# Kernel optimization log

Measured on AMD Instinct MI355X. Metric: run time of the kernel, lower is better.

The kernel has to match this reference:

```python
import jax, jax.numpy as jnp
import numpy as np

N = 50000      # nodes
E = 800000     # edges (avg degree 16)
D = 128        # in_dim == hidden_dim
CD = 3         # coord_dim (SE(3))
L = 3          # num_layers


def setup_inputs() -> dict:
    key = jax.random.key(0)
    ks = jax.random.split(key, 10)
    s = np.float32(1.0 / np.sqrt(D))
    return {
        "x": jax.random.normal(ks[0], (N, D), jnp.float32),
        "pos": jax.random.normal(ks[1], (N, CD), jnp.float32),
        "edge_index": jax.random.randint(ks[2], (2, E), 0, N, dtype=jnp.int32),
        # per-layer stacked params (in_dim == hidden_dim so all layers stack)
        "Wl": jax.random.normal(ks[3], (L, D, D), jnp.float32) * s,
        "bl": jnp.zeros((L, D), jnp.float32),
        "Wc": jax.random.normal(ks[4], (L, D, 1), jnp.float32) * s,
        "bc": jnp.zeros((L, 1), jnp.float32),
        "WR": jax.random.normal(ks[5], (L, D, CD * CD), jnp.float32) * s,
        "bR": jnp.zeros((L, CD * CD), jnp.float32),
        "Wt": jax.random.normal(ks[6], (L, D, CD), jnp.float32) * s,
        "bt": jnp.zeros((L, CD), jnp.float32),
        # final fc
        "Wf": jax.random.normal(ks[7], (D, D), jnp.float32) * s,
        "bf": jnp.zeros((D,), jnp.float32),
    }


def reference(x, pos, edge_index, Wl, bl, Wc, bc, WR, bR, Wt, bt, Wf, bf):
    src, dst = edge_index[0], edge_index[1]
    n = x.shape[0]
    # R defaults to identity, t to zeros (R_dict/t_dict None path)
    R = jnp.broadcast_to(jnp.eye(CD, dtype=x.dtype), (n, CD, CD))
    t = jnp.zeros_like(pos)
    for i in range(L):
        h = x @ Wl[i] + bl[i]                          # (N, D)  per-edge-type linear
        # MessagePassing aggr='add': message x_j = h[src], scatter-add at dst
        out = jax.ops.segment_sum(h[src], dst, num_segments=n)  # (N, D)
        pos = pos + (out @ Wc[i] + bc[i])              # (N,3) + (N,1) broadcast
        R_upd = (out @ WR[i] + bR[i]).reshape(n, CD, CD)
        Q = jnp.linalg.qr(R_upd)[0]                    # orthonormalize rotation update
        R = Q @ R
        t = t + (out @ Wt[i] + bt[i])
        x = out
    z = x @ Wf + bf
    return z, pos, R, t
```

## Files before the change

### kernel.cpp

```cpp
#include <hip/hip_runtime.h>
#include <hip/hip_fp16.h>

typedef _Float16 half8 __attribute__((ext_vector_type(8)));
typedef float floatx4 __attribute__((ext_vector_type(4)));

#define NHC 16
#define WCOLS (128 + NHC)
#define OSH 13

__device__ inline void qr3_q(const double A[3][3], double Q[3][3]){
  double a[3][3];
#pragma unroll
  for (int r = 0; r < 3; r++)
#pragma unroll
    for (int c = 0; c < 3; c++) a[r][c] = A[r][c];

  double v1[3] = {1.0, 0.0, 0.0};
  double tau1 = 0.0;
  {
    double xn2 = a[1][0]*a[1][0] + a[2][0]*a[2][0];
    if (xn2 != 0.0){
      double alpha = a[0][0];
      double beta = -copysign(sqrt(alpha*alpha + xn2), alpha);
      tau1 = (beta - alpha) / beta;
      double inv = 1.0 / (alpha - beta);
      v1[1] = a[1][0] * inv;
      v1[2] = a[2][0] * inv;
#pragma unroll
      for (int c = 1; c < 3; c++){
        double w = a[0][c] + v1[1]*a[1][c] + v1[2]*a[2][c];
        double tw = tau1 * w;
        a[0][c] -= tw;
        a[1][c] -= tw * v1[1];
        a[2][c] -= tw * v1[2];
      }
    }
  }
  double tau2 = 0.0, v2 = 0.0;
  {
    double x2 = a[2][1];
    if (x2 != 0.0){
      double alpha = a[1][1];
      double beta = -copysign(sqrt(alpha*alpha + x2*x2), alpha);
      tau2 = (beta - alpha) / beta;
      v2 = x2 / (alpha - beta);
    }
  }
  double M[3][3] = {{1.0, 0.0, 0.0},
                    {0.0, 1.0 - tau2, -tau2*v2},
                    {0.0, -tau2*v2, 1.0 - tau2*v2*v2}};
#pragma unroll
  for (int c = 0; c < 3; c++){
    double w = v1[0]*M[0][c] + v1[1]*M[1][c] + v1[2]*M[2][c];
#pragma unroll
    for (int r = 0; r < 3; r++)
      Q[r][c] = M[r][c] - tau1 * v1[r] * w;
  }
}

__device__ inline void se3_node(int n, const float* __restrict__ dsws,
                                const float* __restrict__ bc, const float* __restrict__ bR,
                                const float* __restrict__ bt, const float* __restrict__ pos_in,
                                float* __restrict__ pos_o, float* __restrict__ R_o,
                                float* __restrict__ t_o, int layer, int N){
  float ds[13];
#pragma unroll
  for (int c = 0; c < 13; c++) ds[c] = dsws[(size_t)c*N + n];

  double A[3][3], Q[3][3];
#pragma unroll
  for (int r = 0; r < 3; r++)
#pragma unroll
    for (int c = 0; c < 3; c++)
      A[r][c] = (double)ds[1 + r*3 + c] + (double)bR[r*3 + c];
  qr3_q(A, Q);

  double pd = (double)ds[0] + (double)bc[0];
#pragma unroll
  for (int c = 0; c < 3; c++){
    double base = (layer == 0) ? (double)pos_in[n*3 + c] : (double)pos_o[n*3 + c];
    pos_o[n*3 + c] = (float)(base + pd);
  }

  if (layer == 0){
#pragma unroll
    for (int r = 0; r < 3; r++)
#pragma unroll
      for (int c = 0; c < 3; c++)
        R_o[n*9 + r*3 + c] = (float)Q[r][c];
  } else {
    double Rold[3][3];
#pragma unroll
    for (int r = 0; r < 3; r++)
#pragma unroll
      for (int c = 0; c < 3; c++)
        Rold[r][c] = (double)R_o[n*9 + r*3 + c];
#pragma unroll
    for (int r = 0; r < 3; r++)
#pragma unroll
      for (int c = 0; c < 3; c++){
        double s = Q[r][0]*Rold[0][c] + Q[r][1]*Rold[1][c] + Q[r][2]*Rold[2][c];
        R_o[n*9 + r*3 + c] = (float)s;
      }
  }
#pragma unroll
  for (int c = 0; c < 3; c++){
    double base = (layer == 0) ? 0.0 : (double)t_o[n*3 + c];
    t_o[n*3 + c] = (float)(base + (double)ds[10 + c] + (double)bt[c]);
  }
}

__global__ void k_prep_w(const float* __restrict__ Wl, const float* __restrict__ Wf,
                         const float* __restrict__ Wc, const float* __restrict__ WR,
                         const float* __restrict__ Wt, _Float16* __restrict__ wTx,
                         int* __restrict__ cursor, int nbuck){
  int t = blockIdx.x*256 + threadIdx.x;
  if (blockIdx.x == 0 && threadIdx.x < nbuck) cursor[threadIdx.x] = 0;
  if (t >= 4*WCOLS*128) return;
  int l = t / (WCOLS*128);
  int rem = t - l*(WCOLS*128);
  int n = rem >> 7;
  int k = rem & 127;
  float v = 0.f;
  if (n < 128){
    const float* W = (l < 3) ? (Wl + (size_t)l*16384) : Wf;
    v = W[k*128 + n];
  } else if (l > 0){
    int h = n - 128, hl = l - 1;
    if (h == 0)       v = Wc[(size_t)hl*128 + k];
    else if (h < 10)  v = WR[(size_t)hl*128*9 + k*9 + (h-1)];
    else if (h < 13)  v = Wt[(size_t)hl*128*3 + k*3 + (h-10)];
  }
  wTx[t] = (_Float16)v;
}

__launch_bounds__(256)
__global__ void k_bin(const int* __restrict__ src, const int* __restrict__ dst,
                      int E, int nbuck, int capB,
                      int* __restrict__ cursor, int* __restrict__ binned){
  __shared__ int cnt[128];
  __shared__ int segbase[128];
  const int tid = threadIdx.x;
  for (int t = tid; t < nbuck; t += 256) cnt[t] = 0;
  __syncthreads();
  const int e0 = blockIdx.x*4096 + tid;
  int pk[16], bk[16];
#pragma unroll
  for (int j = 0; j < 16; j++){
    int e = e0 + j*256;
    if (e < E){
      int d = dst[e], s = src[e];
      bk[j] = d >> 9;
      pk[j] = (s << 9) | (d & 511);
      atomicAdd(&cnt[bk[j]], 1);
    } else bk[j] = -1;
  }
  __syncthreads();
  for (int t = tid; t < nbuck; t += 256){
    int c = cnt[t];
    if (c > 0) segbase[t] = t*capB + atomicAdd(&cursor[t], c);
    cnt[t] = 0;
  }
  __syncthreads();
#pragma unroll
  for (int j = 0; j < 16; j++){
    if (bk[j] >= 0){
      int ord = atomicAdd(&cnt[bk[j]], 1);
      binned[segbase[bk[j]] + ord] = pk[j];
    }
  }
}

__launch_bounds__(256)
__global__ void k_build(const int* __restrict__ binned, const int* __restrict__ cursor,
                        int N, int capB, int capC,
                        int2* __restrict__ sd, int* __restrict__ csr){
  __shared__ int deg2[512*8];
  __shared__ int lst2[512*8];
  __shared__ int cnt2[512*8];
  __shared__ int scn[256];
  const int b = blockIdx.x, tid = threadIdx.x;
  for (int t = tid; t < 512*8; t += 256){ deg2[t] = 0; cnt2[t] = 0; }
  __syncthreads();
  const int nE = cursor[b];
  const int gbase = b*capB;
  for (int i = tid; i < nE; i += 256){
    int v = binned[gbase + i];
    int o = v >> (9 + OSH);
    if (o > 7) o = 7;
    atomicAdd(&deg2[((v & 511) << 3) + o], 1);
  }
  __syncthreads();
  int d0 = 0, d1 = 0;
#pragma unroll
  for (int o = 0; o < 8; o++){ d0 += deg2[((2*tid) << 3) + o]; d1 += deg2[((2*tid+1) << 3) + o]; }
  const int p0 = (d0+7)&~7, p1 = (d1+7)&~7;
  scn[tid] = p0 + p1;
  __syncthreads();
#pragma unroll
  for (int off = 1; off < 256; off <<= 1){
    int add = (tid >= off) ? scn[tid-off] : 0;
    __syncthreads();
    scn[tid] += add;
    __syncthreads();
  }
  const int ex = scn[tid] - (p0 + p1);
  const int csrb = b*capC;
  {
    int off0 = ex;
#pragma unroll
    for (int o = 0; o < 8; o++){ lst2[((2*tid) << 3) + o] = off0; off0 += deg2[((2*tid) << 3) + o]; }
    int off1 = ex + p0;
#pragma unroll
    for (int o = 0; o < 8; o++){ lst2[((2*tid+1) << 3) + o] = off1; off1 += deg2[((2*tid+1) << 3) + o]; }
  }
  const int n0 = b*512 + 2*tid, n1 = n0 + 1;
  if (n0 < N) sd[n0] = make_int2(csrb + ex, p0);
  if (n1 < N) sd[n1] = make_int2(csrb + ex + p0, p1);
  __syncthreads();
  for (int i = tid; i < nE; i += 256){
    int v = binned[gbase + i];
    int dl = v & 511, s = v >> 9;
    int o = s >> OSH; if (o > 7) o = 7;
    int ord = atomicAdd(&cnt2[(dl << 3) + o], 1);
    csr[csrb + lst2[(dl << 3) + o] + ord] = s;
  }
  for (int j = d0; j < p0; j++) csr[csrb + ex + j] = N;
  for (int j = d1; j < p1; j++) csr[csrb + ex + p0 + j] = N;
}

__launch_bounds__(256)
__global__ void k_gemm_mfma(const void* __restrict__ Xin, const _Float16* __restrict__ Wt,
                            const float* __restrict__ bias, void* __restrict__ Hout,
                            float* __restrict__ dsws,
                            int M, int in_fp32, int out_fp32, int zero_pad){
  const int wave = threadIdx.x >> 6;
  const int lane = threadIdx.x & 63;
  const int quad = lane >> 4;
  const int l16  = lane & 15;
  const int rbase = blockIdx.x*64 + (wave & 1)*32;
  const int cthi = wave >> 1;
  const int ctb = cthi*4;

  const _Float16* X16 = (const _Float16*)Xin;
  const float*    X32 = (const float*)Xin;

  half8 af[4][2];
#pragma unroll
  for (int kc = 0; kc < 4; kc++){
#pragma unroll
    for (int rt = 0; rt < 2; rt++){
      int r = rbase + rt*16 + l16;
      r = (r < M) ? r : (M - 1);
      if (in_fp32){
        const float* p = X32 + (size_t)r*128 + kc*32 + quad*8;
        float4 f0 = *(const float4*)p;
        float4 f1 = *(const float4*)(p + 4);
        half8 a;
        a[0]=(_Float16)f0.x; a[1]=(_Float16)f0.y; a[2]=(_Float16)f0.z; a[3]=(_Float16)f0.w;
        a[4]=(_Float16)f1.x; a[5]=(_Float16)f1.y; a[6]=(_Float16)f1.z; a[7]=(_Float16)f1.w;
        af[kc][rt] = a;
      } else {
        af[kc][rt] = *(const half8*)(X16 + (size_t)r*128 + kc*32 + quad*8);
      }
    }
  }

  floatx4 acc[2][5] = {};
#pragma unroll
  for (int kc = 0; kc < 4; kc++){
#pragma unroll
    for (int ct = 0; ct < 5; ct++){
      if (ct == 4 && cthi == 0) continue;
      half8 bf = *(const half8*)(Wt + (size_t)((ctb+ct)*16 + l16)*128 + kc*32 + quad*8);
      acc[0][ct] = __builtin_amdgcn_mfma_f32_16x16x32_f16(af[kc][0], bf, acc[0][ct], 0, 0, 0);
      acc[1][ct] = __builtin_amdgcn_mfma_f32_16x16x32_f16(af[kc][1], bf, acc[1][ct], 0, 0, 0);
    }
  }
#pragma unroll
  for (int rt = 0; rt < 2; rt++){
#pragma unroll
    for (int ct = 0; ct < 5; ct++){
      if (ct == 4 && cthi == 0) continue;
      int col = (ctb+ct)*16 + l16;
      float bv = (col < 128) ? bias[col] : 0.f;
#pragma unroll
      for (int reg = 0; reg < 4; reg++){
        int r = rbase + rt*16 + quad*4 + reg;
        if (r < M){
          float v = acc[rt][ct][reg] + bv;
          if (col < 128){
            if (out_fp32) ((float*)Hout)[(size_t)r*128 + col] = v;
            else          ((_Float16*)Hout)[(size_t)r*128 + col] = (_Float16)v;
          } else if (col < 141){
            dsws[(size_t)(col-128)*M + r] = v;
          }
        } else if (zero_pad && r == M && !out_fp32 && col < 128){
          ((_Float16*)Hout)[(size_t)r*128 + col] = (_Float16)0.f;
        }
      }
    }
  }
}

__launch_bounds__(256)
__global__ void k_agg(const _Float16* __restrict__ H, const int* __restrict__ csr,
                      const int2* __restrict__ sd, _Float16* __restrict__ Xout,
                      int N, int agg_blocks,
                      const float* __restrict__ dsws, const float* __restrict__ bc,
                      const float* __restrict__ bR, const float* __restrict__ bt,
                      const float* __restrict__ pos_in, float* __restrict__ pos_o,
                      float* __restrict__ R_o, float* __restrict__ t_o, int se3_layer){
  if ((int)blockIdx.x >= agg_blocks){
    int n = (blockIdx.x - agg_blocks)*256 + threadIdx.x;
    if (n < N) se3_node(n, dsws, bc, bR, bt, pos_in, pos_o, R_o, t_o, se3_layer, N);
    return;
  }
  const int wave = threadIdx.x >> 6;
  const int lane = threadIdx.x & 63;
  const int node = blockIdx.x*4 + wave;
  if (node >= N) return;
  int2 s = sd[node];
  const int s0 = s.x, degp = s.y;
  const unsigned int* Hu = (const unsigned int*)H;
  float acc0 = 0.f, acc1 = 0.f;
  for (int base = 0; base < degp; base += 64){
    int myidx = csr[s0 + base + lane];
    int m = degp - base; m = (m < 64) ? m : 64;
    for (int k = 0; k < m; k += 8){
      unsigned int v[8];
#pragma unroll
      for (int j = 0; j < 8; j++){
        int idx = __builtin_amdgcn_readlane(myidx, k + j);
        v[j] = Hu[(size_t)idx*64 + lane];
      }
#pragma unroll
      for (int j = 0; j < 8; j++){
        float2 f = __half22float2(*(__half2*)&v[j]);
        acc0 += f.x; acc1 += f.y;
      }
    }
  }
  __half2 ho = __floats2half2_rn(acc0, acc1);
  ((unsigned int*)Xout)[(size_t)node*64 + lane] = *(unsigned int*)&ho;
}

__launch_bounds__(256)
__global__ void k_se3(const float* __restrict__ dsws,
                      const float* __restrict__ bc, const float* __restrict__ bR,
                      const float* __restrict__ bt, const float* __restrict__ pos_in,
                      float* __restrict__ pos_o, float* __restrict__ R_o, float* __restrict__ t_o,
                      int layer, int N){
  int n = blockIdx.x*256 + threadIdx.x;
  if (n < N) se3_node(n, dsws, bc, bR, bt, pos_in, pos_o, R_o, t_o, layer, N);
}

extern "C" void kernel_launch(void* const* d_in, const int* in_sizes, int n_in,
                              void* d_out, int out_size, void* d_ws, size_t ws_size,
                              hipStream_t stream){
  const float* x0  = (const float*)d_in[0];
  const float* pos = (const float*)d_in[1];
  const int*   ei  = (const int*)d_in[2];
  const float* Wl  = (const float*)d_in[3];
  const float* bl  = (const float*)d_in[4];
  const float* Wc  = (const float*)d_in[5];
  const float* bc  = (const float*)d_in[6];
  const float* WR  = (const float*)d_in[7];
  const float* bR  = (const float*)d_in[8];
  const float* Wt  = (const float*)d_in[9];
  const float* bt  = (const float*)d_in[10];
  const float* Wf  = (const float*)d_in[11];
  const float* bf  = (const float*)d_in[12];

  const int N = in_sizes[0] / 128;
  const int E = in_sizes[2] / 2;
  const int* srcp = ei;
  const int* dstp = ei + E;

  float* z_out = (float*)d_out;
  float* pos_o = z_out + (size_t)N*128;
  float* R_o   = pos_o + (size_t)N*3;
  float* t_o   = R_o   + (size_t)N*9;

  const int nbuck = (N + 511) >> 9;
  const int capB  = (((E + nbuck - 1)/nbuck)*5/4 + 256 + 63) & ~63;
  const int capC  = capB + 512*7;

  char* ws = (char*)d_ws;
  size_t off = 0;
  auto alloc = [&](size_t bytes)->char*{
    char* p = ws + off; off += (bytes + 511) & ~(size_t)511; return p;
  };
  _Float16* buf0h = (_Float16*)alloc((size_t)N*128*2);
  _Float16* buf1h = (_Float16*)alloc((size_t)(N+1)*128*2);
  _Float16* wTx   = (_Float16*)alloc((size_t)4*WCOLS*128*2);
  float* dsws   = (float*)alloc((size_t)13*N*4);
  int2*  sd     = (int2*) alloc((size_t)N*8);
  int*   cursor = (int*)  alloc((size_t)nbuck*4);
  int*   binned = (int*)  alloc((size_t)nbuck*capB*4);
  int*   csr    = (int*)  alloc((size_t)nbuck*capC*4);

  k_prep_w<<<dim3((4*WCOLS*128 + 255)/256), dim3(256), 0, stream>>>(
      Wl, Wf, Wc, WR, Wt, wTx, cursor, nbuck);
  k_bin   <<<dim3((E + 4095)/4096), dim3(256), 0, stream>>>(srcp, dstp, E, nbuck, capB, cursor, binned);
  k_build <<<dim3(nbuck), dim3(256), 0, stream>>>(binned, cursor, N, capB, capC, sd, csr);

  const int gemm_blocks_pad = (N + 64)/64;
  const int gemm_blocks     = (N + 63)/64;
  const int agg_blocks      = (N + 3)/4;
  const int se3_blocks      = (N + 255)/256;

  const void* xcur = (const void*)x0;
  for (int layer = 0; layer < 3; layer++){
    k_gemm_mfma<<<dim3(gemm_blocks_pad), dim3(256), 0, stream>>>(
        xcur, wTx + (size_t)layer*WCOLS*128, bl + (size_t)layer*128, (void*)buf1h,
        dsws, N, (layer == 0) ? 1 : 0, 0, 1);
    int extra = (layer >= 1) ? se3_blocks : 0;
    k_agg<<<dim3(agg_blocks + extra), dim3(256), 0, stream>>>(
        buf1h, csr, sd, buf0h, N, agg_blocks,
        dsws, bc + (layer-1), bR + (size_t)(layer-1)*9, bt + (size_t)(layer-1)*3,
        pos, pos_o, R_o, t_o, layer - 1);
    xcur = (const void*)buf0h;
  }
  k_gemm_mfma<<<dim3(gemm_blocks), dim3(256), 0, stream>>>(
      xcur, wTx + (size_t)3*WCOLS*128, bf, (void*)z_out, dsws, N, 0, 1, 0);
  k_se3<<<dim3(se3_blocks), dim3(256), 0, stream>>>(
      dsws, bc + 2, bR + 18, bt + 6, pos, pos_o, R_o, t_o, 2, N);
}
```

Before: 318.7 us.

## Fuse SE3 head processing into GEMM epilogue and stage outputs through LDS

The GEMM epilogue now writes results into shared memory and then stores them with vectorized row-contiguous writes instead of scattered per-element stores. The 13 head columns (pos/rotation/translation projections) stay in LDS, and one wave per block runs the QR/SE3 node update directly. This removes the dsws global scratch buffer, the extra se3 blocks in k_agg and the final k_se3 launch. The costs are about 36KB of LDS per block, which may lower occupancy, and a serial double-precision QR tail on a single wave inside the GEMM.

```diff
diff --git a/kernel.cpp b/kernel.cpp
--- a/kernel.cpp
+++ b/kernel.cpp
@@ -58,15 +58,11 @@
   }
 }
 
-__device__ inline void se3_node(int n, const float* __restrict__ dsws,
-                                const float* __restrict__ bc, const float* __restrict__ bR,
-                                const float* __restrict__ bt, const float* __restrict__ pos_in,
-                                float* __restrict__ pos_o, float* __restrict__ R_o,
-                                float* __restrict__ t_o, int layer, int N){
-  float ds[13];
-#pragma unroll
-  for (int c = 0; c < 13; c++) ds[c] = dsws[(size_t)c*N + n];
-
+__device__ inline void se3_node_ds(int n, const float ds[13],
+                                   const float* __restrict__ bc, const float* __restrict__ bR,
+                                   const float* __restrict__ bt, const float* __restrict__ pos_in,
+                                   float* __restrict__ pos_o, float* __restrict__ R_o,
+                                   float* __restrict__ t_o, int layer){
   double A[3][3], Q[3][3];
 #pragma unroll
   for (int r = 0; r < 3; r++)
@@ -232,13 +228,24 @@
 __launch_bounds__(256)
 __global__ void k_gemm_mfma(const void* __restrict__ Xin, const _Float16* __restrict__ Wt,
                             const float* __restrict__ bias, void* __restrict__ Hout,
-                            float* __restrict__ dsws,
-                            int M, int in_fp32, int out_fp32, int zero_pad){
-  const int wave = threadIdx.x >> 6;
-  const int lane = threadIdx.x & 63;
+                            int M, int in_fp32, int out_fp32, int zero_pad,
+                            int se3_layer,
+                            const float* __restrict__ bc, const float* __restrict__ bR,
+                            const float* __restrict__ bt, const float* __restrict__ pos_in,
+                            float* __restrict__ pos_o, float* __restrict__ R_o,
+                            float* __restrict__ t_o, int N){
+  __shared__ __align__(16) unsigned char lds[64*128*4 + 64*16*4];
+  _Float16* lh = (_Float16*)lds;
+  float*    lf = (float*)lds;
+  float*    lheads = (float*)(lds + 64*128*4);
+
+  const int tid  = threadIdx.x;
+  const int wave = tid >> 6;
+  const int lane = tid & 63;
   const int quad = lane >> 4;
   const int l16  = lane & 15;
-  const int rbase = blockIdx.x*64 + (wave & 1)*32;
+  const int rbase0 = blockIdx.x*64;
+  const int rbase  = rbase0 + (wave & 1)*32;
   const int cthi = wave >> 1;
   const int ctb = cthi*4;
 
@@ -277,45 +284,67 @@
       acc[1][ct] = __builtin_amdgcn_mfma_f32_16x16x32_f16(af[kc][1], bf, acc[1][ct], 0, 0, 0);
     }
   }
+
 #pragma unroll
   for (int rt = 0; rt < 2; rt++){
 #pragma unroll
     for (int ct = 0; ct < 5; ct++){
       if (ct == 4 && cthi == 0) continue;
       int col = (ctb+ct)*16 + l16;
-      float bv = (col < 128) ? bias[col] : 0.f;
 #pragma unroll
       for (int reg = 0; reg < 4; reg++){
-        int r = rbase + rt*16 + quad*4 + reg;
-        if (r < M){
-          float v = acc[rt][ct][reg] + bv;
-          if (col < 128){
-            if (out_fp32) ((float*)Hout)[(size_t)r*128 + col] = v;
-            else          ((_Float16*)Hout)[(size_t)r*128 + col] = (_Float16)v;
-          } else if (col < 141){
-            dsws[(size_t)(col-128)*M + r] = v;
-          }
-        } else if (zero_pad && r == M && !out_fp32 && col < 128){
-          ((_Float16*)Hout)[(size_t)r*128 + col] = (_Float16)0.f;
+        int rl = (wave & 1)*32 + rt*16 + quad*4 + reg;
+        float v = acc[rt][ct][reg];
+        if (col < 128){
+          v += bias[col];
+          if (out_fp32) lf[rl*128 + col] = v;
+          else          lh[rl*128 + col] = (_Float16)v;
+        } else {
+          lheads[rl*16 + (col - 128)] = v;
         }
       }
+    }
+  }
+  __syncthreads();
+
+  if (out_fp32){
+#pragma unroll
+    for (int i = 0; i < 8; i++){
+      int idx4 = i*256 + tid;
+      int row = idx4 >> 5, c4 = idx4 & 31;
+      int gr = rbase0 + row;
+      if (gr < M)
+        *(float4*)((float*)Hout + (size_t)gr*128 + c4*4) = *(const float4*)&lf[row*128 + c4*4];
+    }
+  } else {
+#pragma unroll
+    for (int i = 0; i < 4; i++){
+      int idx8 = i*256 + tid;
+      int row = idx8 >> 4, c8 = idx8 & 15;
+      int gr = rbase0 + row;
+      if (gr < M){
+        *(half8*)((_Float16*)Hout + (size_t)gr*128 + c8*8) = *(const half8*)&lh[row*128 + c8*8];
+      } else if (zero_pad && gr == M){
+        half8 z = {};
+        *(half8*)((_Float16*)Hout + (size_t)gr*128 + c8*8) = z;
+      }
+    }
+  }
+
+  if (se3_layer >= 0 && tid < 64){
+    int n = rbase0 + tid;
+    if (n < N){
+      float ds[13];
+#pragma unroll
+      for (int c = 0; c < 13; c++) ds[c] = lheads[tid*16 + c];
+      se3_node_ds(n, ds, bc, bR, bt, pos_in, pos_o, R_o, t_o, se3_layer);
     }
   }
 }
 
 __launch_bounds__(256)
 __global__ void k_agg(const _Float16* __restrict__ H, const int* __restrict__ csr,
-                      const int2* __restrict__ sd, _Float16* __restrict__ Xout,
-                      int N, int agg_blocks,
-                      const float* __restrict__ dsws, const float* __restrict__ bc,
-                      const float* __restrict__ bR, const float* __restrict__ bt,
-                      const float* __restrict__ pos_in, float* __restrict__ pos_o,
-                      float* __restrict__ R_o, float* __restrict__ t_o, int se3_layer){
-  if ((int)blockIdx.x >= agg_blocks){
-    int n = (blockIdx.x - agg_blocks)*256 + threadIdx.x;
-    if (n < N) se3_node(n, dsws, bc, bR, bt, pos_in, pos_o, R_o, t_o, se3_layer, N);
-    return;
-  }
+                      const int2* __restrict__ sd, _Float16* __restrict__ Xout, int N){
   const int wave = threadIdx.x >> 6;
   const int lane = threadIdx.x & 63;
   const int node = blockIdx.x*4 + wave;
@@ -343,16 +372,6 @@
   }
   __half2 ho = __floats2half2_rn(acc0, acc1);
   ((unsigned int*)Xout)[(size_t)node*64 + lane] = *(unsigned int*)&ho;
-}
-
-__launch_bounds__(256)
-__global__ void k_se3(const float* __restrict__ dsws,
-                      const float* __restrict__ bc, const float* __restrict__ bR,
-                      const float* __restrict__ bt, const float* __restrict__ pos_in,
-                      float* __restrict__ pos_o, float* __restrict__ R_o, float* __restrict__ t_o,
-                      int layer, int N){
-  int n = blockIdx.x*256 + threadIdx.x;
-  if (n < N) se3_node(n, dsws, bc, bR, bt, pos_in, pos_o, R_o, t_o, layer, N);
 }
 
 extern "C" void kernel_launch(void* const* d_in, const int* in_sizes, int n_in,
@@ -394,7 +413,6 @@
   _Float16* buf0h = (_Float16*)alloc((size_t)N*128*2);
   _Float16* buf1h = (_Float16*)alloc((size_t)(N+1)*128*2);
   _Float16* wTx   = (_Float16*)alloc((size_t)4*WCOLS*128*2);
-  float* dsws   = (float*)alloc((size_t)13*N*4);
   int2*  sd     = (int2*) alloc((size_t)N*8);
   int*   cursor = (int*)  alloc((size_t)nbuck*4);
   int*   binned = (int*)  alloc((size_t)nbuck*capB*4);
@@ -408,22 +426,20 @@
   const int gemm_blocks_pad = (N + 64)/64;
   const int gemm_blocks     = (N + 63)/64;
   const int agg_blocks      = (N + 3)/4;
-  const int se3_blocks      = (N + 255)/256;
 
   const void* xcur = (const void*)x0;
   for (int layer = 0; layer < 3; layer++){
     k_gemm_mfma<<<dim3(gemm_blocks_pad), dim3(256), 0, stream>>>(
         xcur, wTx + (size_t)layer*WCOLS*128, bl + (size_t)layer*128, (void*)buf1h,
-        dsws, N, (layer == 0) ? 1 : 0, 0, 1);
-    int extra = (layer >= 1) ? se3_blocks : 0;
-    k_agg<<<dim3(agg_blocks + extra), dim3(256), 0, stream>>>(
-        buf1h, csr, sd, buf0h, N, agg_blocks,
-        dsws, bc + (layer-1), bR + (size_t)(layer-1)*9, bt + (size_t)(layer-1)*3,
-        pos, pos_o, R_o, t_o, layer - 1);
+        N, (layer == 0) ? 1 : 0, 0, 1,
+        layer - 1, bc + (layer-1), bR + (size_t)(layer-1)*9, bt + (size_t)(layer-1)*3,
+        pos, pos_o, R_o, t_o, N);
+    k_agg<<<dim3(agg_blocks), dim3(256), 0, stream>>>(buf1h, csr, sd, buf0h, N);
     xcur = (const void*)buf0h;
   }
   k_gemm_mfma<<<dim3(gemm_blocks), dim3(256), 0, stream>>>(
-      xcur, wTx + (size_t)3*WCOLS*128, bf, (void*)z_out, dsws, N, 0, 1, 0);
-  k_se3<<<dim3(se3_blocks), dim3(256), 0, stream>>>(
-      dsws, bc + 2, bR + 18, bt + 6, pos, pos_o, R_o, t_o, 2, N);
-}
+      xcur, wTx + (size_t)3*WCOLS*128, bf, (void*)z_out,
+      N, 0, 1, 0,
+      2, bc + 2, bR + 18, bt + 6,
+      pos, pos_o, R_o, t_o, N);
+}
```

After: 305.1 us. 4.3% less time.
